# Performance work log

Hardware: AMD Instinct MI355X
Metric: run time of the kernel (lower is better)

## Reference

```python
import jax, jax.numpy as jnp
import numpy as np

D = 1024
H = 16
HD = D // H
FF = 4 * D
EPS = 1e-5


def setup_inputs() -> dict:
    key = jax.random.key(0)
    ks = jax.random.split(key, 16)
    s = lambda k, shape, scale: jax.random.normal(k, shape, dtype=jnp.float32) * scale
    inp = {
        "x": s(ks[0], (8, 1024, D), 1.0),
        "Wq": s(ks[1], (D, D), D ** -0.5), "bq": jnp.zeros((D,), jnp.float32),
        "Wk": s(ks[2], (D, D), D ** -0.5), "bk": jnp.zeros((D,), jnp.float32),
        "Wv": s(ks[3], (D, D), D ** -0.5), "bv": jnp.zeros((D,), jnp.float32),
        "Wo": s(ks[4], (D, D), D ** -0.5), "bo": jnp.zeros((D,), jnp.float32),
        "W1": s(ks[5], (D, FF), D ** -0.5), "b1": jnp.zeros((FF,), jnp.float32),
        "W2": s(ks[6], (FF, D), FF ** -0.5), "b2": jnp.zeros((D,), jnp.float32),
        "g1": jnp.ones((D,), jnp.float32), "be1": jnp.zeros((D,), jnp.float32),
        "g2": jnp.ones((D,), jnp.float32), "be2": jnp.zeros((D,), jnp.float32),
    }
    return inp


def _layernorm(x, g, b):
    mu = jnp.mean(x, axis=-1, keepdims=True)
    var = jnp.var(x, axis=-1, keepdims=True)
    return (x - mu) * jax.lax.rsqrt(var + EPS) * g + b


def reference(x, Wq, bq, Wk, bk, Wv, bv, Wo, bo, W1, b1, W2, b2, g1, be1, g2, be2):
    B, S, _ = x.shape
    # --- pre-norm attention block (dropout = identity in eval) ---
    h = _layernorm(x, g1, be1)
    q = (h @ Wq + bq).reshape(B, S, H, HD)
    k = (h @ Wk + bk).reshape(B, S, H, HD)
    v = (h @ Wv + bv).reshape(B, S, H, HD)
    scores = jnp.einsum('bqhd,bkhd->bhqk', q, k) / jnp.sqrt(jnp.float32(HD))
    attn = jax.nn.softmax(scores, axis=-1)
    ctx = jnp.einsum('bhqk,bkhd->bqhd', attn, v).reshape(B, S, D)
    x = x + (ctx @ Wo + bo)
    # --- pre-norm FFN block ---
    h = _layernorm(x, g2, be2)
    h = jax.nn.gelu(h @ W1 + b1, approximate=False)
    x = x + (h @ W2 + b2)
    return x
```

## Files before the change

### kernel.cpp

```cpp
#include <hip/hip_runtime.h>
#include <hip/hip_bf16.h>
#include <math.h>
#include <stdint.h>

typedef unsigned short u16;
typedef unsigned int u32;
typedef __attribute__((ext_vector_type(8))) short short8;
typedef __attribute__((ext_vector_type(4))) float f32x4;

__device__ __forceinline__ float b2f(u16 u) {
  union { u32 i; float f; } v; v.i = ((u32)u) << 16; return v.f;
}
__device__ __forceinline__ u16 f2b(float f) {
  union { float f; u32 i; } v; v.f = f;
  return (u16)((v.i + 0x7FFFu + ((v.i >> 16) & 1u)) >> 16);
}

__device__ __forceinline__ void gload_lds16(const u16* g, u16* l) {
  __builtin_amdgcn_global_load_lds((const __attribute__((address_space(1))) void*)g,
                                   (__attribute__((address_space(3))) void*)l, 16, 0, 0);
}

#define LD8(p) (*(const short8*)(p))
#define MFMA_BF16 __builtin_amdgcn_mfma_f32_16x16x32_bf16

__global__ __launch_bounds__(256) void transpose_k(const float* __restrict__ in,
                                                   u16* __restrict__ out, int K, int N) {
  __shared__ u16 tile[32][33];
  int n0 = blockIdx.x * 32, k0 = blockIdx.y * 32;
  int tx = threadIdx.x & 31, ty = threadIdx.x >> 5;
  #pragma unroll
  for (int i = ty; i < 32; i += 8)
    tile[i][tx] = f2b(in[(size_t)(k0 + i) * N + n0 + tx]);
  __syncthreads();
  #pragma unroll
  for (int i = ty; i < 32; i += 8)
    out[(size_t)(n0 + i) * K + k0 + tx] = tile[tx][i];
}

__global__ __launch_bounds__(256) void cat3_k(const float* __restrict__ a, const float* __restrict__ b,
                                              const float* __restrict__ c, float* __restrict__ o) {
  int i = blockIdx.x * 256 + threadIdx.x;
  o[i] = i < 1024 ? a[i] : (i < 2048 ? b[i - 1024] : c[i - 2048]);
}

__global__ __launch_bounds__(256) void vtrans_k(const u16* __restrict__ qkv, u16* __restrict__ vt) {
  __shared__ u16 tile[32][33];
  int bh = blockIdx.y, b = bh >> 4, h = bh & 15;
  int s0 = (blockIdx.x & 31) * 32, d0 = (blockIdx.x >> 5) * 32;
  int tx = threadIdx.x & 31, ty = threadIdx.x >> 5;
  #pragma unroll
  for (int i = ty; i < 32; i += 8)
    tile[i][tx] = qkv[(size_t)(b * 1024 + s0 + i) * 3072 + 2048 + h * 64 + d0 + tx];
  __syncthreads();
  #pragma unroll
  for (int i = ty; i < 32; i += 8)
    vt[(size_t)(bh * 64 + d0 + i) * 1024 + s0 + tx] = tile[tx][i];
}

template<int FP32IN>
__global__ __launch_bounds__(256) void ln_k(const void* __restrict__ xv, const float* __restrict__ g,
                                            const float* __restrict__ be, u16* __restrict__ out) {
  int row = blockIdx.x, t = threadIdx.x;
  float f0, f1, f2, f3;
  if (FP32IN) {
    const float* xr = (const float*)xv + (size_t)row * 1024;
    float4 x4 = *(const float4*)(xr + t * 4);
    f0 = x4.x; f1 = x4.y; f2 = x4.z; f3 = x4.w;
  } else {
    const u16* xr = (const u16*)xv + (size_t)row * 1024;
    ushort4 x4 = *(const ushort4*)(xr + t * 4);
    f0 = b2f(x4.x); f1 = b2f(x4.y); f2 = b2f(x4.z); f3 = b2f(x4.w);
  }
  float s = f0 + f1 + f2 + f3;
  float ss = f0 * f0 + f1 * f1 + f2 * f2 + f3 * f3;
  #pragma unroll
  for (int off = 32; off > 0; off >>= 1) { s += __shfl_down(s, off); ss += __shfl_down(ss, off); }
  __shared__ float sb[4], ssb[4];
  if ((t & 63) == 0) { sb[t >> 6] = s; ssb[t >> 6] = ss; }
  __syncthreads();
  s = sb[0] + sb[1] + sb[2] + sb[3];
  ss = ssb[0] + ssb[1] + ssb[2] + ssb[3];
  float mu = s * (1.0f / 1024.0f);
  float var = ss * (1.0f / 1024.0f) - mu * mu;
  float rstd = rsqrtf(var + 1e-5f);
  float4 gv = *(const float4*)(g + t * 4);
  float4 bv = *(const float4*)(be + t * 4);
  ushort4 o;
  o.x = f2b((f0 - mu) * rstd * gv.x + bv.x);
  o.y = f2b((f1 - mu) * rstd * gv.y + bv.y);
  o.z = f2b((f2 - mu) * rstd * gv.z + bv.z);
  o.w = f2b((f3 - mu) * rstd * gv.w + bv.w);
  *(ushort4*)(out + (size_t)row * 1024 + t * 4) = o;
}

template<int ACT, int RESID, int OUTF32>
__global__ __launch_bounds__(512, 2) void gemm256_k(const u16* __restrict__ A, const u16* __restrict__ Bt,
                                                    const float* __restrict__ bias, const void* __restrict__ resid,
                                                    void* __restrict__ Cv, int M, int N, int K, int ldc) {
  __shared__ u16 As[2][256 * 64];
  __shared__ u16 Bs[2][256 * 64];
  int Ny = N >> 8;
  int lin = blockIdx.y * 32 + blockIdx.x;
  int c8 = lin & 7, sblk = lin >> 3;
  int mq = sblk / Ny;
  int m0 = ((mq << 3) | c8) << 8;
  int n0 = (sblk - mq * Ny) << 8;
  int t = threadIdx.x;
  int wave = t >> 6, lane = t & 63, quad = lane >> 4, l16 = lane & 15;
  int wm = (wave >> 2) << 7;
  int wn = (wave & 3) << 6;
  f32x4 acc[8][4] = {};
  int lrow = lane >> 3;
  int lchunk = (lane & 7) ^ lrow;
  const u16* Ab = A + (size_t)(m0 + wave * 32 + lrow) * K + lchunk * 8;
  const u16* Bb = Bt + (size_t)(n0 + wave * 32 + lrow) * K + lchunk * 8;
  const int sbase = wave * 32 * 64;
  const int x7 = l16 & 7;
  const int rdA = (wm + l16) * 64;
  const int rdB = (wn + l16) * 64;
  const int cz0 = (quad ^ x7) * 8;
  const int cz1 = ((4 + quad) ^ x7) * 8;
  const int niter = K >> 6;
  #pragma unroll
  for (int g = 0; g < 4; g++) {
    gload_lds16(Ab + (size_t)g * 8 * K, &As[0][sbase + g * 8 * 64]);
    gload_lds16(Bb + (size_t)g * 8 * K, &Bs[0][sbase + g * 8 * 64]);
  }
  asm volatile("s_waitcnt vmcnt(0)" ::: "memory");
  __builtin_amdgcn_s_barrier();
  __builtin_amdgcn_sched_barrier(0);
  for (int tt = 0; tt < niter; tt++) {
    int buf = tt & 1;
    const bool pf = (tt + 1 < niter);
    const int kpf = (tt + 1) << 6;
    const u16* Ac = &As[buf][0];
    const u16* Bc = &Bs[buf][0];
    u16* Aw = &As[buf ^ 1][0];
    u16* Bw = &Bs[buf ^ 1][0];
    short8 a0, a1, a2, a3, a4, a5, a6, a7, b0, b1, b2, b3;
    a0 = LD8(Ac + rdA + cz0);
    a1 = LD8(Ac + rdA + 1024 + cz0);
    a2 = LD8(Ac + rdA + 2048 + cz0);
    a3 = LD8(Ac + rdA + 3072 + cz0);
    b0 = LD8(Bc + rdB + cz0);
    b1 = LD8(Bc + rdB + 1024 + cz0);
    b2 = LD8(Bc + rdB + 2048 + cz0);
    b3 = LD8(Bc + rdB + 3072 + cz0);
    if (pf) {
      #pragma unroll
      for (int g = 0; g < 4; g++)
        gload_lds16(Ab + kpf + (size_t)g * 8 * K, Aw + sbase + g * 8 * 64);
    }
    __builtin_amdgcn_s_barrier();
    asm volatile("s_waitcnt lgkmcnt(0)" ::: "memory");
    __builtin_amdgcn_sched_barrier(0);
    __builtin_amdgcn_s_setprio(1);
    acc[0][0] = MFMA_BF16(a0, b0, acc[0][0], 0, 0, 0);
    acc[0][1] = MFMA_BF16(a0, b1, acc[0][1], 0, 0, 0);
    acc[0][2] = MFMA_BF16(a0, b2, acc[0][2], 0, 0, 0);
    acc[0][3] = MFMA_BF16(a0, b3, acc[0][3], 0, 0, 0);
    acc[1][0] = MFMA_BF16(a1, b0, acc[1][0], 0, 0, 0);
    acc[1][1] = MFMA_BF16(a1, b1, acc[1][1], 0, 0, 0);
    acc[1][2] = MFMA_BF16(a1, b2, acc[1][2], 0, 0, 0);
    acc[1][3] = MFMA_BF16(a1, b3, acc[1][3], 0, 0, 0);
    acc[2][0] = MFMA_BF16(a2, b0, acc[2][0], 0, 0, 0);
    acc[2][1] = MFMA_BF16(a2, b1, acc[2][1], 0, 0, 0);
    acc[2][2] = MFMA_BF16(a2, b2, acc[2][2], 0, 0, 0);
    acc[2][3] = MFMA_BF16(a2, b3, acc[2][3], 0, 0, 0);
    acc[3][0] = MFMA_BF16(a3, b0, acc[3][0], 0, 0, 0);
    acc[3][1] = MFMA_BF16(a3, b1, acc[3][1], 0, 0, 0);
    acc[3][2] = MFMA_BF16(a3, b2, acc[3][2], 0, 0, 0);
    acc[3][3] = MFMA_BF16(a3, b3, acc[3][3], 0, 0, 0);
    __builtin_amdgcn_s_setprio(0);
    __builtin_amdgcn_s_barrier();
    __builtin_amdgcn_sched_barrier(0);
    a4 = LD8(Ac + rdA + 4096 + cz0);
    a5 = LD8(Ac + rdA + 5120 + cz0);
    a6 = LD8(Ac + rdA + 6144 + cz0);
    a7 = LD8(Ac + rdA + 7168 + cz0);
    if (pf) {
      #pragma unroll
      for (int g = 0; g < 4; g++)
        gload_lds16(Bb + kpf + (size_t)g * 8 * K, Bw + sbase + g * 8 * 64);
    }
    __builtin_amdgcn_s_barrier();
    asm volatile("s_waitcnt lgkmcnt(0)" ::: "memory");
    __builtin_amdgcn_sched_barrier(0);
    __builtin_amdgcn_s_setprio(1);
    acc[4][0] = MFMA_BF16(a4, b0, acc[4][0], 0, 0, 0);
    acc[4][1] = MFMA_BF16(a4, b1, acc[4][1], 0, 0, 0);
    acc[4][2] = MFMA_BF16(a4, b2, acc[4][2], 0, 0, 0);
    acc[4][3] = MFMA_BF16(a4, b3, acc[4][3], 0, 0, 0);
    acc[5][0] = MFMA_BF16(a5, b0, acc[5][0], 0, 0, 0);
    acc[5][1] = MFMA_BF16(a5, b1, acc[5][1], 0, 0, 0);
    acc[5][2] = MFMA_BF16(a5, b2, acc[5][2], 0, 0, 0);
    acc[5][3] = MFMA_BF16(a5, b3, acc[5][3], 0, 0, 0);
    acc[6][0] = MFMA_BF16(a6, b0, acc[6][0], 0, 0, 0);
    acc[6][1] = MFMA_BF16(a6, b1, acc[6][1], 0, 0, 0);
    acc[6][2] = MFMA_BF16(a6, b2, acc[6][2], 0, 0, 0);
    acc[6][3] = MFMA_BF16(a6, b3, acc[6][3], 0, 0, 0);
    acc[7][0] = MFMA_BF16(a7, b0, acc[7][0], 0, 0, 0);
    acc[7][1] = MFMA_BF16(a7, b1, acc[7][1], 0, 0, 0);
    acc[7][2] = MFMA_BF16(a7, b2, acc[7][2], 0, 0, 0);
    acc[7][3] = MFMA_BF16(a7, b3, acc[7][3], 0, 0, 0);
    __builtin_amdgcn_s_setprio(0);
    __builtin_amdgcn_s_barrier();
    __builtin_amdgcn_sched_barrier(0);
    a0 = LD8(Ac + rdA + cz1);
    a1 = LD8(Ac + rdA + 1024 + cz1);
    a2 = LD8(Ac + rdA + 2048 + cz1);
    a3 = LD8(Ac + rdA + 3072 + cz1);
    b0 = LD8(Bc + rdB + cz1);
    b1 = LD8(Bc + rdB + 1024 + cz1);
    b2 = LD8(Bc + rdB + 2048 + cz1);
    b3 = LD8(Bc + rdB + 3072 + cz1);
    __builtin_amdgcn_s_barrier();
    asm volatile("s_waitcnt lgkmcnt(0)" ::: "memory");
    __builtin_amdgcn_sched_barrier(0);
    __builtin_amdgcn_s_setprio(1);
    acc[0][0] = MFMA_BF16(a0, b0, acc[0][0], 0, 0, 0);
    acc[0][1] = MFMA_BF16(a0, b1, acc[0][1], 0, 0, 0);
    acc[0][2] = MFMA_BF16(a0, b2, acc[0][2], 0, 0, 0);
    acc[0][3] = MFMA_BF16(a0, b3, acc[0][3], 0, 0, 0);
    acc[1][0] = MFMA_BF16(a1, b0, acc[1][0], 0, 0, 0);
    acc[1][1] = MFMA_BF16(a1, b1, acc[1][1], 0, 0, 0);
    acc[1][2] = MFMA_BF16(a1, b2, acc[1][2], 0, 0, 0);
    acc[1][3] = MFMA_BF16(a1, b3, acc[1][3], 0, 0, 0);
    acc[2][0] = MFMA_BF16(a2, b0, acc[2][0], 0, 0, 0);
    acc[2][1] = MFMA_BF16(a2, b1, acc[2][1], 0, 0, 0);
    acc[2][2] = MFMA_BF16(a2, b2, acc[2][2], 0, 0, 0);
    acc[2][3] = MFMA_BF16(a2, b3, acc[2][3], 0, 0, 0);
    acc[3][0] = MFMA_BF16(a3, b0, acc[3][0], 0, 0, 0);
    acc[3][1] = MFMA_BF16(a3, b1, acc[3][1], 0, 0, 0);
    acc[3][2] = MFMA_BF16(a3, b2, acc[3][2], 0, 0, 0);
    acc[3][3] = MFMA_BF16(a3, b3, acc[3][3], 0, 0, 0);
    __builtin_amdgcn_s_setprio(0);
    __builtin_amdgcn_s_barrier();
    __builtin_amdgcn_sched_barrier(0);
    a4 = LD8(Ac + rdA + 4096 + cz1);
    a5 = LD8(Ac + rdA + 5120 + cz1);
    a6 = LD8(Ac + rdA + 6144 + cz1);
    a7 = LD8(Ac + rdA + 7168 + cz1);
    __builtin_amdgcn_s_barrier();
    asm volatile("s_waitcnt lgkmcnt(0)" ::: "memory");
    __builtin_amdgcn_sched_barrier(0);
    __builtin_amdgcn_s_setprio(1);
    acc[4][0] = MFMA_BF16(a4, b0, acc[4][0], 0, 0, 0);
    acc[4][1] = MFMA_BF16(a4, b1, acc[4][1], 0, 0, 0);
    acc[4][2] = MFMA_BF16(a4, b2, acc[4][2], 0, 0, 0);
    acc[4][3] = MFMA_BF16(a4, b3, acc[4][3], 0, 0, 0);
    acc[5][0] = MFMA_BF16(a5, b0, acc[5][0], 0, 0, 0);
    acc[5][1] = MFMA_BF16(a5, b1, acc[5][1], 0, 0, 0);
    acc[5][2] = MFMA_BF16(a5, b2, acc[5][2], 0, 0, 0);
    acc[5][3] = MFMA_BF16(a5, b3, acc[5][3], 0, 0, 0);
    acc[6][0] = MFMA_BF16(a6, b0, acc[6][0], 0, 0, 0);
    acc[6][1] = MFMA_BF16(a6, b1, acc[6][1], 0, 0, 0);
    acc[6][2] = MFMA_BF16(a6, b2, acc[6][2], 0, 0, 0);
    acc[6][3] = MFMA_BF16(a6, b3, acc[6][3], 0, 0, 0);
    acc[7][0] = MFMA_BF16(a7, b0, acc[7][0], 0, 0, 0);
    acc[7][1] = MFMA_BF16(a7, b1, acc[7][1], 0, 0, 0);
    acc[7][2] = MFMA_BF16(a7, b2, acc[7][2], 0, 0, 0);
    acc[7][3] = MFMA_BF16(a7, b3, acc[7][3], 0, 0, 0);
    __builtin_amdgcn_s_setprio(0);
    if (pf) {
      asm volatile("s_waitcnt vmcnt(0)" ::: "memory");
      __builtin_amdgcn_s_barrier();
      __builtin_amdgcn_sched_barrier(0);
    }
  }
  float bcol[4];
  #pragma unroll
  for (int j = 0; j < 4; j++) bcol[j] = bias[n0 + wn + j * 16 + l16];
  #pragma unroll
  for (int i = 0; i < 8; i++) {
    #pragma unroll
    for (int r = 0; r < 4; r++) {
      int row = m0 + wm + i * 16 + quad * 4 + r;
      #pragma unroll
      for (int j = 0; j < 4; j++) {
        int col = n0 + wn + j * 16 + l16;
        float v = acc[i][j][r] + bcol[j];
        if (ACT == 1) {
          float e = v * (2.3022082f + 0.1029431f * v * v);
          float tt2 = exp2f(fminf(e, 80.0f));
          v = v * tt2 / (tt2 + 1.0f);
        }
        if (RESID == 1) v += b2f(((const u16*)resid)[(size_t)row * N + col]);
        if (RESID == 2) v += ((const float*)resid)[(size_t)row * N + col];
        if (OUTF32) ((float*)Cv)[(size_t)row * ldc + col] = v;
        else        ((u16*)Cv)[(size_t)row * ldc + col] = f2b(v);
      }
    }
  }
}

template<int ACT, int RESID, int OUTF32>
__global__ __launch_bounds__(512, 2) void gemm256n_k(const u16* __restrict__ A, const u16* __restrict__ Bt,
                                                     const float* __restrict__ bias, const void* __restrict__ resid,
                                                     void* __restrict__ Cv, int M, int N, int K, int ldc) {
  __shared__ u16 As[3][256 * 64];
  __shared__ u16 Bs[3][128 * 64];
  int Ny = N >> 7;
  int lin = blockIdx.y * 32 + blockIdx.x;
  int c8 = lin & 7, sblk = lin >> 3;
  int mq = sblk / Ny;
  int m0 = ((mq << 3) | c8) << 8;
  int n0 = (sblk - mq * Ny) << 7;
  int t = threadIdx.x;
  int wave = t >> 6, lane = t & 63, quad = lane >> 4, l16 = lane & 15;
  int wm = (wave >> 1) << 6;
  int wn = (wave & 1) << 6;
  f32x4 acc[4][4] = {};
  int lrow = lane >> 3;
  int lchunk = (lane & 7) ^ lrow;
  const u16* Ab = A + (size_t)(m0 + wave * 32 + lrow) * K + lchunk * 8;
  const u16* Bb = Bt + (size_t)(n0 + wave * 16 + lrow) * K + lchunk * 8;
  const int sbA = wave * 32 * 64;
  const int sbB = wave * 16 * 64;
  const int x7 = l16 & 7;
  const int rdA = (wm + l16) * 64;
  const int rdB = (wn + l16) * 64;
  const int cz0 = (quad ^ x7) * 8;
  const int cz1 = ((4 + quad) ^ x7) * 8;
  const int niter = K >> 6;
  #pragma unroll
  for (int p = 0; p < 2; p++) {
    #pragma unroll
    for (int g = 0; g < 4; g++)
      gload_lds16(Ab + (p << 6) + (size_t)g * 8 * K, &As[p][sbA + g * 8 * 64]);
    #pragma unroll
    for (int g = 0; g < 2; g++)
      gload_lds16(Bb + (p << 6) + (size_t)g * 8 * K, &Bs[p][sbB + g * 8 * 64]);
  }
  asm volatile("s_waitcnt vmcnt(6)" ::: "memory");
  __builtin_amdgcn_s_barrier();
  __builtin_amdgcn_sched_barrier(0);
  int cur = 0;
  for (int tt = 0; tt < niter; tt++) {
    int wb = cur + 2; if (wb >= 3) wb -= 3;
    const bool pf = (tt + 2 < niter);
    const int kpf = (tt + 2) << 6;
    const u16* Ac = &As[cur][0];
    const u16* Bc = &Bs[cur][0];
    short8 a0, a1, a2, a3, b0, b1, b2, b3;
    a0 = LD8(Ac + rdA + cz0);
    a1 = LD8(Ac + rdA + 1024 + cz0);
    a2 = LD8(Ac + rdA + 2048 + cz0);
    a3 = LD8(Ac + rdA + 3072 + cz0);
    b0 = LD8(Bc + rdB + cz0);
    b1 = LD8(Bc + rdB + 1024 + cz0);
    b2 = LD8(Bc + rdB + 2048 + cz0);
    b3 = LD8(Bc + rdB + 3072 + cz0);
    if (pf) {
      #pragma unroll
      for (int g = 0; g < 4; g++)
        gload_lds16(Ab + kpf + (size_t)g * 8 * K, &As[wb][sbA + g * 8 * 64]);
    }
    __builtin_amdgcn_s_barrier();
    asm volatile("s_waitcnt lgkmcnt(0)" ::: "memory");
    __builtin_amdgcn_sched_barrier(0);
    __builtin_amdgcn_s_setprio(1);
    acc[0][0] = MFMA_BF16(a0, b0, acc[0][0], 0, 0, 0);
    acc[0][1] = MFMA_BF16(a0, b1, acc[0][1], 0, 0, 0);
    acc[0][2] = MFMA_BF16(a0, b2, acc[0][2], 0, 0, 0);
    acc[0][3] = MFMA_BF16(a0, b3, acc[0][3], 0, 0, 0);
    acc[1][0] = MFMA_BF16(a1, b0, acc[1][0], 0, 0, 0);
    acc[1][1] = MFMA_BF16(a1, b1, acc[1][1], 0, 0, 0);
    acc[1][2] = MFMA_BF16(a1, b2, acc[1][2], 0, 0, 0);
    acc[1][3] = MFMA_BF16(a1, b3, acc[1][3], 0, 0, 0);
    acc[2][0] = MFMA_BF16(a2, b0, acc[2][0], 0, 0, 0);
    acc[2][1] = MFMA_BF16(a2, b1, acc[2][1], 0, 0, 0);
    acc[2][2] = MFMA_BF16(a2, b2, acc[2][2], 0, 0, 0);
    acc[2][3] = MFMA_BF16(a2, b3, acc[2][3], 0, 0, 0);
    acc[3][0] = MFMA_BF16(a3, b0, acc[3][0], 0, 0, 0);
    acc[3][1] = MFMA_BF16(a3, b1, acc[3][1], 0, 0, 0);
    acc[3][2] = MFMA_BF16(a3, b2, acc[3][2], 0, 0, 0);
    acc[3][3] = MFMA_BF16(a3, b3, acc[3][3], 0, 0, 0);
    __builtin_amdgcn_s_setprio(0);
    __builtin_amdgcn_s_barrier();
    __builtin_amdgcn_sched_barrier(0);
    a0 = LD8(Ac + rdA + cz1);
    a1 = LD8(Ac + rdA + 1024 + cz1);
    a2 = LD8(Ac + rdA + 2048 + cz1);
    a3 = LD8(Ac + rdA + 3072 + cz1);
    b0 = LD8(Bc + rdB + cz1);
    b1 = LD8(Bc + rdB + 1024 + cz1);
    b2 = LD8(Bc + rdB + 2048 + cz1);
    b3 = LD8(Bc + rdB + 3072 + cz1);
    if (pf) {
      #pragma unroll
      for (int g = 0; g < 2; g++)
        gload_lds16(Bb + kpf + (size_t)g * 8 * K, &Bs[wb][sbB + g * 8 * 64]);
    }
    __builtin_amdgcn_s_barrier();
    asm volatile("s_waitcnt lgkmcnt(0)" ::: "memory");
    __builtin_amdgcn_sched_barrier(0);
    __builtin_amdgcn_s_setprio(1);
    acc[0][0] = MFMA_BF16(a0, b0, acc[0][0], 0, 0, 0);
    acc[0][1] = MFMA_BF16(a0, b1, acc[0][1], 0, 0, 0);
    acc[0][2] = MFMA_BF16(a0, b2, acc[0][2], 0, 0, 0);
    acc[0][3] = MFMA_BF16(a0, b3, acc[0][3], 0, 0, 0);
    acc[1][0] = MFMA_BF16(a1, b0, acc[1][0], 0, 0, 0);
    acc[1][1] = MFMA_BF16(a1, b1, acc[1][1], 0, 0, 0);
    acc[1][2] = MFMA_BF16(a1, b2, acc[1][2], 0, 0, 0);
    acc[1][3] = MFMA_BF16(a1, b3, acc[1][3], 0, 0, 0);
    acc[2][0] = MFMA_BF16(a2, b0, acc[2][0], 0, 0, 0);
    acc[2][1] = MFMA_BF16(a2, b1, acc[2][1], 0, 0, 0);
    acc[2][2] = MFMA_BF16(a2, b2, acc[2][2], 0, 0, 0);
    acc[2][3] = MFMA_BF16(a2, b3, acc[2][3], 0, 0, 0);
    acc[3][0] = MFMA_BF16(a3, b0, acc[3][0], 0, 0, 0);
    acc[3][1] = MFMA_BF16(a3, b1, acc[3][1], 0, 0, 0);
    acc[3][2] = MFMA_BF16(a3, b2, acc[3][2], 0, 0, 0);
    acc[3][3] = MFMA_BF16(a3, b3, acc[3][3], 0, 0, 0);
    __builtin_amdgcn_s_setprio(0);
    if (tt + 2 < niter) {
      asm volatile("s_waitcnt vmcnt(6)" ::: "memory");
    } else if (tt + 1 < niter) {
      asm volatile("s_waitcnt vmcnt(0)" ::: "memory");
    }
    if (tt + 1 < niter) {
      __builtin_amdgcn_s_barrier();
      __builtin_amdgcn_sched_barrier(0);
    }
    cur = (cur == 2) ? 0 : cur + 1;
  }
  float bcol[4];
  #pragma unroll
  for (int j = 0; j < 4; j++) bcol[j] = bias[n0 + wn + j * 16 + l16];
  #pragma unroll
  for (int i = 0; i < 4; i++) {
    #pragma unroll
    for (int r = 0; r < 4; r++) {
      int row = m0 + wm + i * 16 + quad * 4 + r;
      #pragma unroll
      for (int j = 0; j < 4; j++) {
        int col = n0 + wn + j * 16 + l16;
        float v = acc[i][j][r] + bcol[j];
        if (ACT == 1) {
          float e = v * (2.3022082f + 0.1029431f * v * v);
          float tt2 = exp2f(fminf(e, 80.0f));
          v = v * tt2 / (tt2 + 1.0f);
        }
        if (RESID == 1) v += b2f(((const u16*)resid)[(size_t)row * N + col]);
        if (RESID == 2) v += ((const float*)resid)[(size_t)row * N + col];
        if (OUTF32) ((float*)Cv)[(size_t)row * ldc + col] = v;
        else        ((u16*)Cv)[(size_t)row * ldc + col] = f2b(v);
      }
    }
  }
}

__global__ __launch_bounds__(256) void attn_k(const u16* __restrict__ QKV, const u16* __restrict__ VT,
                                              u16* __restrict__ ctx) {
  int bh = blockIdx.x;
  int b = bh >> 4;
  int q0 = blockIdx.y * 64;
  int t = threadIdx.x, wave = t >> 6, lane = t & 63, quad = lane >> 4, l16 = lane & 15;
  __shared__ u16 Ks[2][64 * 64];
  __shared__ u16 Vs[2][64 * 64];
  __shared__ u16 Plds[4][16][72];
  const size_t base = ((size_t)b * 1024) * 3072 + (size_t)(bh & 15) * 64;
  const u16* Kbase = QKV + base + 1024;
  const u16* vtb = VT + (size_t)bh * 64 * 1024;
  int lrow = lane >> 3;
  int lchunk = (lane & 7) ^ (lrow & 7);
  int srow = wave * 16;
  short8 qa[2];
  #pragma unroll
  for (int kh = 0; kh < 2; kh++)
    qa[kh] = *(const short8*)(QKV + base + (size_t)(q0 + wave * 16 + l16) * 3072 + kh * 32 + quad * 8);
  #pragma unroll
  for (int half = 0; half < 2; half++) {
    int r8 = srow + half * 8;
    gload_lds16(Kbase + (size_t)(r8 + lrow) * 3072 + lchunk * 8, &Ks[0][r8 * 64]);
    gload_lds16(vtb + (size_t)(r8 + lrow) * 1024 + lchunk * 8, &Vs[0][r8 * 64]);
  }
  f32x4 o[4] = {};
  float l_acc[4] = {0.f, 0.f, 0.f, 0.f};
  for (int c = 0; c < 16; c++) {
    int buf = c & 1;
    __syncthreads();
    if (c < 15) {
      #pragma unroll
      for (int half = 0; half < 2; half++) {
        int r8 = srow + half * 8;
        gload_lds16(Kbase + (size_t)((c + 1) * 64 + r8 + lrow) * 3072 + lchunk * 8, &Ks[buf ^ 1][r8 * 64]);
        gload_lds16(vtb + (size_t)(r8 + lrow) * 1024 + (c + 1) * 64 + lchunk * 8, &Vs[buf ^ 1][r8 * 64]);
      }
    }
    f32x4 s[4] = {};
    #pragma unroll
    for (int kh = 0; kh < 2; kh++)
      #pragma unroll
      for (int j = 0; j < 4; j++) {
        int row = j * 16 + l16;
        int pc = (kh * 4 + quad) ^ (row & 7);
        short8 kb = *(const short8*)(&Ks[buf][row * 64 + pc * 8]);
        s[j] = MFMA_BF16(qa[kh], kb, s[j], 0, 0, 0);
      }
    #pragma unroll
    for (int j = 0; j < 4; j++)
      #pragma unroll
      for (int r = 0; r < 4; r++) {
        float p = exp2f(s[j][r] * 0.18033688011112042f);
        l_acc[r] += p;
        Plds[wave][quad * 4 + r][j * 16 + l16] = f2b(p);
      }
    #pragma unroll
    for (int kh = 0; kh < 2; kh++) {
      short8 pa = *(const short8*)(&Plds[wave][l16][kh * 32 + quad * 8]);
      #pragma unroll
      for (int d4 = 0; d4 < 4; d4++) {
        int row = d4 * 16 + l16;
        int pc = (kh * 4 + quad) ^ (row & 7);
        short8 vb = *(const short8*)(&Vs[buf][row * 64 + pc * 8]);
        o[d4] = MFMA_BF16(pa, vb, o[d4], 0, 0, 0);
      }
    }
  }
  #pragma unroll
  for (int off = 1; off < 16; off <<= 1)
    #pragma unroll
    for (int r = 0; r < 4; r++) l_acc[r] += __shfl_xor(l_acc[r], off);
  #pragma unroll
  for (int r = 0; r < 4; r++) {
    float inv = 1.0f / l_acc[r];
    size_t row = (size_t)b * 1024 + q0 + wave * 16 + quad * 4 + r;
    #pragma unroll
    for (int d4 = 0; d4 < 4; d4++) {
      int col = (bh & 15) * 64 + d4 * 16 + l16;
      ctx[row * 1024 + col] = f2b(o[d4][r] * inv);
    }
  }
}

extern "C" void kernel_launch(void* const* d_in, const int* in_sizes, int n_in,
                              void* d_out, int out_size, void* d_ws, size_t ws_size,
                              hipStream_t stream) {
  const float* x   = (const float*)d_in[0];
  const float* Wq  = (const float*)d_in[1];  const float* bq  = (const float*)d_in[2];
  const float* Wk  = (const float*)d_in[3];  const float* bk  = (const float*)d_in[4];
  const float* Wv  = (const float*)d_in[5];  const float* bv  = (const float*)d_in[6];
  const float* Wo  = (const float*)d_in[7];  const float* bo  = (const float*)d_in[8];
  const float* W1  = (const float*)d_in[9];  const float* b1  = (const float*)d_in[10];
  const float* W2  = (const float*)d_in[11]; const float* b2  = (const float*)d_in[12];
  const float* g1  = (const float*)d_in[13]; const float* be1 = (const float*)d_in[14];
  const float* g2  = (const float*)d_in[15]; const float* be2 = (const float*)d_in[16];

  char* ws = (char*)d_ws;
  const size_t MB = 1024 * 1024;
  u16* h1    = (u16*)(ws + 0 * MB);
  u16* qkv   = (u16*)(ws + 16 * MB);
  u16* x1    = (u16*)(ws + 16 * MB);
  u16* h2    = (u16*)(ws + 32 * MB);
  u16* W2T   = (u16*)(ws + 48 * MB);
  u16* WqkvT = (u16*)(ws + 64 * MB);
  u16* WoT   = (u16*)(ws + 70 * MB);
  u16* W1T   = (u16*)(ws + 72 * MB);
  float* bqkv = (float*)(ws + 80 * MB);
  u16* h3f   = (u16*)(ws + 80 * MB);
  u16* vt    = h1;
  u16* ctx   = (u16*)d_out;
  float* out = (float*)d_out;

  transpose_k<<<dim3(32, 32), 256, 0, stream>>>(Wq, WqkvT, 1024, 1024);
  transpose_k<<<dim3(32, 32), 256, 0, stream>>>(Wk, WqkvT + (size_t)1024 * 1024, 1024, 1024);
  transpose_k<<<dim3(32, 32), 256, 0, stream>>>(Wv, WqkvT + (size_t)2048 * 1024, 1024, 1024);
  transpose_k<<<dim3(32, 32), 256, 0, stream>>>(Wo, WoT, 1024, 1024);
  transpose_k<<<dim3(128, 32), 256, 0, stream>>>(W1, W1T, 1024, 4096);
  cat3_k<<<12, 256, 0, stream>>>(bq, bk, bv, bqkv);

  ln_k<1><<<8192, 256, 0, stream>>>(x, g1, be1, h1);

  gemm256_k<0, 0, 0><<<dim3(32, 12), 512, 0, stream>>>(h1, WqkvT, bqkv, nullptr, qkv,
                                                       8192, 3072, 1024, 3072);

  vtrans_k<<<dim3(64, 128), 256, 0, stream>>>(qkv, vt);

  attn_k<<<dim3(128, 16), 256, 0, stream>>>(qkv, vt, ctx);

  gemm256n_k<0, 2, 0><<<dim3(32, 8), 512, 0, stream>>>(ctx, WoT, bo, x, x1,
                                                       8192, 1024, 1024, 1024);

  transpose_k<<<dim3(32, 128), 256, 0, stream>>>(W2, W2T, 4096, 1024);

  ln_k<0><<<8192, 256, 0, stream>>>(x1, g2, be2, h2);

  gemm256_k<1, 0, 0><<<dim3(32, 16), 512, 0, stream>>>(h2, W1T, b1, nullptr, h3f,
                                                       8192, 4096, 1024, 4096);
  gemm256n_k<0, 1, 1><<<dim3(32, 8), 512, 0, stream>>>(h3f, W2T, b2, x1, out,
                                                       8192, 1024, 4096, 1024);

  (void)in_sizes; (void)n_in; (void)out_size; (void)ws_size;
}
```

Measured before the change: 515.4 us.

## Triple-buffer K/V tiles in attention with explicit vmcnt waits and setprio

```diff
diff --git a/kernel.cpp b/kernel.cpp
--- a/kernel.cpp
+++ b/kernel.cpp
@@ -457,8 +457,8 @@
   int b = bh >> 4;
   int q0 = blockIdx.y * 64;
   int t = threadIdx.x, wave = t >> 6, lane = t & 63, quad = lane >> 4, l16 = lane & 15;
-  __shared__ u16 Ks[2][64 * 64];
-  __shared__ u16 Vs[2][64 * 64];
+  __shared__ u16 Ks[3][64 * 64];
+  __shared__ u16 Vs[3][64 * 64];
   __shared__ u16 Plds[4][16][72];
   const size_t base = ((size_t)b * 1024) * 3072 + (size_t)(bh & 15) * 64;
   const u16* Kbase = QKV + base + 1024;
@@ -471,34 +471,46 @@
   for (int kh = 0; kh < 2; kh++)
     qa[kh] = *(const short8*)(QKV + base + (size_t)(q0 + wave * 16 + l16) * 3072 + kh * 32 + quad * 8);
   #pragma unroll
-  for (int half = 0; half < 2; half++) {
-    int r8 = srow + half * 8;
-    gload_lds16(Kbase + (size_t)(r8 + lrow) * 3072 + lchunk * 8, &Ks[0][r8 * 64]);
-    gload_lds16(vtb + (size_t)(r8 + lrow) * 1024 + lchunk * 8, &Vs[0][r8 * 64]);
+  for (int p = 0; p < 2; p++) {
+    #pragma unroll
+    for (int half = 0; half < 2; half++) {
+      int r8 = srow + half * 8;
+      gload_lds16(Kbase + (size_t)(p * 64 + r8 + lrow) * 3072 + lchunk * 8, &Ks[p][r8 * 64]);
+      gload_lds16(vtb + (size_t)(r8 + lrow) * 1024 + p * 64 + lchunk * 8, &Vs[p][r8 * 64]);
+    }
   }
   f32x4 o[4] = {};
   float l_acc[4] = {0.f, 0.f, 0.f, 0.f};
+  int cur = 0;
   for (int c = 0; c < 16; c++) {
-    int buf = c & 1;
-    __syncthreads();
     if (c < 15) {
+      asm volatile("s_waitcnt vmcnt(4)" ::: "memory");
+    } else {
+      asm volatile("s_waitcnt vmcnt(0)" ::: "memory");
+    }
+    __builtin_amdgcn_s_barrier();
+    __builtin_amdgcn_sched_barrier(0);
+    if (c + 2 < 16) {
+      int wb = cur + 2; if (wb >= 3) wb -= 3;
       #pragma unroll
       for (int half = 0; half < 2; half++) {
         int r8 = srow + half * 8;
-        gload_lds16(Kbase + (size_t)((c + 1) * 64 + r8 + lrow) * 3072 + lchunk * 8, &Ks[buf ^ 1][r8 * 64]);
-        gload_lds16(vtb + (size_t)(r8 + lrow) * 1024 + (c + 1) * 64 + lchunk * 8, &Vs[buf ^ 1][r8 * 64]);
+        gload_lds16(Kbase + (size_t)((c + 2) * 64 + r8 + lrow) * 3072 + lchunk * 8, &Ks[wb][r8 * 64]);
+        gload_lds16(vtb + (size_t)(r8 + lrow) * 1024 + (c + 2) * 64 + lchunk * 8, &Vs[wb][r8 * 64]);
       }
     }
     f32x4 s[4] = {};
+    __builtin_amdgcn_s_setprio(1);
     #pragma unroll
     for (int kh = 0; kh < 2; kh++)
       #pragma unroll
       for (int j = 0; j < 4; j++) {
         int row = j * 16 + l16;
         int pc = (kh * 4 + quad) ^ (row & 7);
-        short8 kb = *(const short8*)(&Ks[buf][row * 64 + pc * 8]);
+        short8 kb = *(const short8*)(&Ks[cur][row * 64 + pc * 8]);
         s[j] = MFMA_BF16(qa[kh], kb, s[j], 0, 0, 0);
       }
+    __builtin_amdgcn_s_setprio(0);
     #pragma unroll
     for (int j = 0; j < 4; j++)
       #pragma unroll
@@ -507,6 +519,7 @@
         l_acc[r] += p;
         Plds[wave][quad * 4 + r][j * 16 + l16] = f2b(p);
       }
+    __builtin_amdgcn_s_setprio(1);
     #pragma unroll
     for (int kh = 0; kh < 2; kh++) {
       short8 pa = *(const short8*)(&Plds[wave][l16][kh * 32 + quad * 8]);
@@ -514,10 +527,12 @@
       for (int d4 = 0; d4 < 4; d4++) {
         int row = d4 * 16 + l16;
         int pc = (kh * 4 + quad) ^ (row & 7);
-        short8 vb = *(const short8*)(&Vs[buf][row * 64 + pc * 8]);
+        short8 vb = *(const short8*)(&Vs[cur][row * 64 + pc * 8]);
         o[d4] = MFMA_BF16(pa, vb, o[d4], 0, 0, 0);
       }
     }
+    __builtin_amdgcn_s_setprio(0);
+    cur = (cur == 2) ? 0 : cur + 1;
   }
   #pragma unroll
   for (int off = 1; off < 16; off <<= 1)
```

Measured after the change: 534.6 us. 3.7% more time.

## Double attention query tile per block to 128 rows with 8 waves

Applied to the files above, without the earlier changes.

```diff
diff --git a/kernel.cpp b/kernel.cpp
--- a/kernel.cpp
+++ b/kernel.cpp
@@ -451,43 +451,35 @@
   }
 }
 
-__global__ __launch_bounds__(256) void attn_k(const u16* __restrict__ QKV, const u16* __restrict__ VT,
+__global__ __launch_bounds__(512) void attn_k(const u16* __restrict__ QKV, const u16* __restrict__ VT,
                                               u16* __restrict__ ctx) {
   int bh = blockIdx.x;
   int b = bh >> 4;
-  int q0 = blockIdx.y * 64;
+  int q0 = blockIdx.y * 128;
   int t = threadIdx.x, wave = t >> 6, lane = t & 63, quad = lane >> 4, l16 = lane & 15;
   __shared__ u16 Ks[2][64 * 64];
   __shared__ u16 Vs[2][64 * 64];
-  __shared__ u16 Plds[4][16][72];
+  __shared__ u16 Plds[8][16][72];
   const size_t base = ((size_t)b * 1024) * 3072 + (size_t)(bh & 15) * 64;
   const u16* Kbase = QKV + base + 1024;
   const u16* vtb = VT + (size_t)bh * 64 * 1024;
   int lrow = lane >> 3;
-  int lchunk = (lane & 7) ^ (lrow & 7);
-  int srow = wave * 16;
+  int lchunk = (lane & 7) ^ lrow;
+  int srow = wave * 8;
   short8 qa[2];
   #pragma unroll
   for (int kh = 0; kh < 2; kh++)
     qa[kh] = *(const short8*)(QKV + base + (size_t)(q0 + wave * 16 + l16) * 3072 + kh * 32 + quad * 8);
-  #pragma unroll
-  for (int half = 0; half < 2; half++) {
-    int r8 = srow + half * 8;
-    gload_lds16(Kbase + (size_t)(r8 + lrow) * 3072 + lchunk * 8, &Ks[0][r8 * 64]);
-    gload_lds16(vtb + (size_t)(r8 + lrow) * 1024 + lchunk * 8, &Vs[0][r8 * 64]);
-  }
+  gload_lds16(Kbase + (size_t)(srow + lrow) * 3072 + lchunk * 8, &Ks[0][srow * 64]);
+  gload_lds16(vtb + (size_t)(srow + lrow) * 1024 + lchunk * 8, &Vs[0][srow * 64]);
   f32x4 o[4] = {};
   float l_acc[4] = {0.f, 0.f, 0.f, 0.f};
   for (int c = 0; c < 16; c++) {
     int buf = c & 1;
     __syncthreads();
     if (c < 15) {
-      #pragma unroll
-      for (int half = 0; half < 2; half++) {
-        int r8 = srow + half * 8;
-        gload_lds16(Kbase + (size_t)((c + 1) * 64 + r8 + lrow) * 3072 + lchunk * 8, &Ks[buf ^ 1][r8 * 64]);
-        gload_lds16(vtb + (size_t)(r8 + lrow) * 1024 + (c + 1) * 64 + lchunk * 8, &Vs[buf ^ 1][r8 * 64]);
-      }
+      gload_lds16(Kbase + (size_t)((c + 1) * 64 + srow + lrow) * 3072 + lchunk * 8, &Ks[buf ^ 1][srow * 64]);
+      gload_lds16(vtb + (size_t)(srow + lrow) * 1024 + (c + 1) * 64 + lchunk * 8, &Vs[buf ^ 1][srow * 64]);
     }
     f32x4 s[4] = {};
     #pragma unroll
@@ -502,10 +494,15 @@
     #pragma unroll
     for (int j = 0; j < 4; j++)
       #pragma unroll
-      for (int r = 0; r < 4; r++) {
-        float p = exp2f(s[j][r] * 0.18033688011112042f);
-        l_acc[r] += p;
-        Plds[wave][quad * 4 + r][j * 16 + l16] = f2b(p);
+      for (int rp = 0; rp < 4; rp += 2) {
+        float p0 = exp2f(s[j][rp]     * 0.18033688011112042f);
+        float p1 = exp2f(s[j][rp + 1] * 0.18033688011112042f);
+        l_acc[rp] += p0;
+        l_acc[rp + 1] += p1;
+        u32 pk;
+        asm("v_cvt_pk_bf16_f32 %0, %1, %2" : "=v"(pk) : "v"(p0), "v"(p1));
+        Plds[wave][quad * 4 + rp][j * 16 + l16]     = (u16)pk;
+        Plds[wave][quad * 4 + rp + 1][j * 16 + l16] = (u16)(pk >> 16);
       }
     #pragma unroll
     for (int kh = 0; kh < 2; kh++) {
@@ -578,7 +575,7 @@
 
   vtrans_k<<<dim3(64, 128), 256, 0, stream>>>(qkv, vt);
 
-  attn_k<<<dim3(128, 16), 256, 0, stream>>>(qkv, vt, ctx);
+  attn_k<<<dim3(128, 8), 512, 0, stream>>>(qkv, vt, ctx);
 
   gemm256n_k<0, 2, 0><<<dim3(32, 8), 512, 0, stream>>>(ctx, WoT, bo, x, x1,
                                                        8192, 1024, 1024, 1024);
```

Result: faster. 496.2 us (-3.7%).
